# Kernel optimization log

Hardware: AMD Instinct MI355X
Metric: run time of the kernel (lower is better)

Reference implementation:

```python
import jax, jax.numpy as jnp
import numpy as np

N_NODES = 50000
N_EDGES = 625000
D = 128


def setup_inputs() -> dict:
    key = jax.random.key(0)
    kx, ks, kr, kw, kb = jax.random.split(key, 5)
    x = jax.random.normal(kx, (N_NODES, D), dtype=jnp.float32)
    senders = jax.random.randint(ks, (N_EDGES,), 0, N_NODES, dtype=jnp.int64)
    receivers = jax.random.randint(kr, (N_EDGES,), 0, N_NODES, dtype=jnp.int64)
    # nn.Linear(2*D, D): weight [D, 2*D], bias [D]
    lim = 1.0 / np.sqrt(2 * D)
    W = jax.random.uniform(kw, (D, 2 * D), minval=-lim, maxval=lim, dtype=jnp.float32)
    b = jax.random.uniform(kb, (D,), minval=-lim, maxval=lim, dtype=jnp.float32)
    return {"x": x, "senders": senders, "receivers": receivers, "n_nodes": N_NODES, "W": W, "b": b}


def reference(x, senders, receivers, n_nodes, W, b):
    # Add self loops (with_self=True)
    self_idx = jnp.arange(n_nodes, dtype=senders.dtype)
    s = jnp.concatenate([senders, self_idx])   # [E + N]
    r = jnp.concatenate([receivers, self_idx]) # [E + N]

    ones = jnp.ones(r.shape[0], dtype=x.dtype)
    # degree_norm=True branch (note: mirrors the original's naming exactly:
    # 'out_degree' counted over receivers, 'in_degree' over senders)
    out_degree = jax.ops.segment_sum(ones, r, num_segments=n_nodes)  # [N]
    in_degree = jax.ops.segment_sum(ones, s, num_segments=n_nodes)   # [N]
    out_degree_norm = jax.lax.rsqrt(jnp.maximum(out_degree, 1.0))
    in_degree_norm = jax.lax.rsqrt(jnp.maximum(in_degree, 1.0))

    # Gather sender embeddings, scale, scatter-add to receivers
    sender_emb = x[s] * out_degree_norm[s][:, None]  # [E+N, D]
    aggregated = jax.ops.segment_sum(sender_emb, r, num_segments=n_nodes)  # [N, D]

    # edge_count over receivers == out_degree (same scatter), clamped
    edge_count = jnp.maximum(out_degree, 1.0)
    aggregated = aggregated / edge_count[:, None]
    aggregated = aggregated * in_degree_norm[:, None]

    combined = jnp.concatenate([x, aggregated], axis=1)  # [N, 2D]
    return combined @ W.T + b
```

## Files before the change

### kernel.cpp

```cpp
#include <hip/hip_runtime.h>

#define DIM 128
#define BM 128
#define BK 32
#define BINSZ 128
#define EPB 2048

typedef __attribute__((ext_vector_type(8))) short short8;
typedef __attribute__((ext_vector_type(4))) float f32x4;

__device__ __forceinline__ unsigned short f2bf(float f) {
    unsigned int b = __float_as_uint(f);
    return (unsigned short)((b + 0x7fffu + ((b >> 16) & 1u)) >> 16);
}
__device__ __forceinline__ float bf_lo(unsigned int u) { return __uint_as_float(u << 16); }
__device__ __forceinline__ float bf_hi(unsigned int u) { return __uint_as_float(u & 0xffff0000u); }
__device__ __forceinline__ unsigned int pack2(float a, float b) {
    return (unsigned int)f2bf(a) | ((unsigned int)f2bf(b) << 16);
}
__device__ __forceinline__ uint2 pack4(float4 v) {
    uint2 r; r.x = pack2(v.x, v.y); r.y = pack2(v.z, v.w); return r;
}

__global__ void convert_kernel(const float4* __restrict__ x4,
                               const float4* __restrict__ W4,
                               uint2* __restrict__ xb4,
                               uint2* __restrict__ Wb4,
                               int nx4, int nw4) {
    int i = blockIdx.x * blockDim.x + threadIdx.x;
    if (i < nx4) xb4[i] = pack4(x4[i]);
    if (i < nw4) Wb4[i] = pack4(W4[i]);
}

__global__ __launch_bounds__(256) void hist_kernel(
        const int* __restrict__ senders, const int* __restrict__ receivers,
        int* __restrict__ Hr, int* __restrict__ Hs, int E, int nbin) {
    __shared__ int hr[512], hs[512];
    int t = threadIdx.x;
    for (int b = t; b < nbin; b += 256) { hr[b] = 0; hs[b] = 0; }
    __syncthreads();
    int base = blockIdx.x * EPB;
    for (int k = 0; k < EPB; k += 256) {
        int e = base + k + t;
        if (e < E) {
            atomicAdd(&hr[receivers[e] >> 7], 1);
            atomicAdd(&hs[senders[e] >> 7], 1);
        }
    }
    __syncthreads();
    size_t ho = (size_t)blockIdx.x * nbin;
    for (int b = t; b < nbin; b += 256) {
        Hr[ho + b] = hr[b];
        Hs[ho + b] = hs[b];
    }
}

__global__ __launch_bounds__(512) void scan_bins_kernel(
        int* __restrict__ Hr, int* __restrict__ Hs,
        int* __restrict__ tot_r, int* __restrict__ tot_s,
        int NAB, int nbin) {
    __shared__ int sr[512], ss[512];
    int b = blockIdx.x, t = threadIdx.x;
    int vr = (t < NAB) ? Hr[(size_t)t * nbin + b] : 0;
    int vs = (t < NAB) ? Hs[(size_t)t * nbin + b] : 0;
    sr[t] = vr; ss[t] = vs;
    __syncthreads();
    for (int off = 1; off < 512; off <<= 1) {
        int ur = (t >= off) ? sr[t - off] : 0;
        int us = (t >= off) ? ss[t - off] : 0;
        __syncthreads();
        sr[t] += ur; ss[t] += us;
        __syncthreads();
    }
    if (t < NAB) {
        Hr[(size_t)t * nbin + b] = sr[t] - vr;
        Hs[(size_t)t * nbin + b] = ss[t] - vs;
    }
    if (t == 511) { tot_r[b] = sr[511]; tot_s[b] = ss[511]; }
}

__global__ __launch_bounds__(512) void scan_base_kernel(
        const int* __restrict__ tot_r, const int* __restrict__ tot_s,
        int* __restrict__ base_r, int* __restrict__ base_s,
        int* __restrict__ row_start, int nbin, int N, int E) {
    __shared__ int sr[512], ss[512];
    int t = threadIdx.x;
    int vr = (t < nbin) ? tot_r[t] : 0;
    int vs = (t < nbin) ? tot_s[t] : 0;
    sr[t] = vr; ss[t] = vs;
    __syncthreads();
    for (int off = 1; off < 512; off <<= 1) {
        int ur = (t >= off) ? sr[t - off] : 0;
        int us = (t >= off) ? ss[t - off] : 0;
        __syncthreads();
        sr[t] += ur; ss[t] += us;
        __syncthreads();
    }
    if (t < nbin) {
        base_r[t] = sr[t] - vr;
        base_s[t] = ss[t] - vs;
    }
    if (t == 0) { base_r[nbin] = E; base_s[nbin] = E; row_start[N] = E; }
}

__global__ __launch_bounds__(256) void scatter_kernel(
        const int* __restrict__ senders, const int* __restrict__ receivers,
        const int* __restrict__ Hr, const int* __restrict__ Hs,
        const int* __restrict__ base_r, const int* __restrict__ base_s,
        unsigned int* __restrict__ bucket_r, int* __restrict__ bucket_s,
        int E, int nbin) {
    __shared__ int br_[512], bs_[512];
    int t = threadIdx.x;
    size_t ho = (size_t)blockIdx.x * nbin;
    for (int b = t; b < nbin; b += 256) {
        br_[b] = base_r[b] + Hr[ho + b];
        bs_[b] = base_s[b] + Hs[ho + b];
    }
    __syncthreads();
    int base = blockIdx.x * EPB;
    for (int k = 0; k < EPB; k += 256) {
        int e = base + k + t;
        if (e < E) {
            int s = senders[e], r = receivers[e];
            int pr = atomicAdd(&br_[r >> 7], 1);
            bucket_r[pr] = ((unsigned int)(r & 127) << 16) | (unsigned int)s;
            int ps = atomicAdd(&bs_[s >> 7], 1);
            bucket_s[ps] = s;
        }
    }
}

__global__ __launch_bounds__(256) void fine_kernel(
        const unsigned int* __restrict__ bucket_r,
        const int* __restrict__ bucket_s,
        const int* __restrict__ base_r,
        const int* __restrict__ base_s,
        const uint2* __restrict__ xb2,
        int* __restrict__ edge_src,
        int* __restrict__ row_start,
        float* __restrict__ fs,
        uint2* __restrict__ xs2,
        int N) {
    __shared__ int fine[BINSZ], fstart[BINSZ], cs[BINSZ];
    __shared__ float scs[BINSZ];
    int b = blockIdx.x, t = threadIdx.x;
    if (t < BINSZ) { fine[t] = 0; cs[t] = 0; }
    __syncthreads();

    int loR = base_r[b], hiR = base_r[b + 1];
    int loS = base_s[b], hiS = base_s[b + 1];
    for (int i = loR + t; i < hiR; i += 256)
        atomicAdd(&fine[bucket_r[i] >> 16], 1);
    for (int i = loS + t; i < hiS; i += 256)
        atomicAdd(&cs[bucket_s[i] & 127], 1);
    __syncthreads();

    if (t < BINSZ) fstart[t] = fine[t];
    __syncthreads();
    for (int off = 1; off < BINSZ; off <<= 1) {
        int u = (t < BINSZ && t >= off) ? fstart[t - off] : 0;
        __syncthreads();
        if (t < BINSZ) fstart[t] += u;
        __syncthreads();
    }
    if (t < BINSZ) {
        int excl = fstart[t] - fine[t];
        int node = b * BINSZ + t;
        float od = (float)(fine[t] + 1);
        float sc = rsqrtf(od);
        scs[t] = sc;
        if (node < N) {
            row_start[node] = loR + excl;
            fs[node] = rsqrtf((float)(cs[t] + 1)) / od;
        }
        fstart[t] = excl;
    }
    __syncthreads();

    for (int i = loR + t; i < hiR; i += 256) {
        unsigned int u = bucket_r[i];
        int pos = atomicAdd(&fstart[u >> 16], 1);
        edge_src[loR + pos] = (int)(u & 0xFFFFu);
    }

    int nrow0 = b * BINSZ;
    for (int idx = t; idx < BINSZ * 32; idx += 256) {
        int row = idx >> 5, c = idx & 31;
        int node = nrow0 + row;
        if (node < N) {
            float sc = scs[row];
            uint2 u = xb2[(size_t)node * 32 + c];
            uint2 o;
            o.x = pack2(bf_lo(u.x) * sc, bf_hi(u.x) * sc);
            o.y = pack2(bf_lo(u.y) * sc, bf_hi(u.y) * sc);
            xs2[(size_t)node * 32 + c] = o;
        }
    }
}

__global__ __launch_bounds__(256) void gather_kernel(
        const unsigned int* __restrict__ xs,
        const int* __restrict__ edge_src,
        const int* __restrict__ row_start,
        const float* __restrict__ fs,
        unsigned int* __restrict__ aggb,
        int N) {
    int lane = threadIdx.x & 63;
    int n = (blockIdx.x * blockDim.x + threadIdx.x) >> 6;
    if (n >= N) return;

    int start = row_start[n];
    int deg   = row_start[n + 1] - start;
    float ax = 0.f, ay = 0.f;

    for (int base = 0; base < deg; base += 64) {
        int cnt = deg - base; if (cnt > 64) cnt = 64;
        int src = 0;
        if (lane < cnt) src = edge_src[start + base + lane];
        int j = 0;
        for (; j + 8 <= cnt; j += 8) {
            int ss[8]; unsigned int uu[8];
#pragma unroll
            for (int q = 0; q < 8; q++) ss[q] = __shfl(src, j + q);
#pragma unroll
            for (int q = 0; q < 8; q++) uu[q] = xs[(size_t)ss[q] * 64 + lane];
#pragma unroll
            for (int q = 0; q < 8; q++) { ax += bf_lo(uu[q]); ay += bf_hi(uu[q]); }
        }
        for (; j < cnt; j++) {
            int s = __shfl(src, j);
            unsigned int u = xs[(size_t)s * 64 + lane];
            ax += bf_lo(u); ay += bf_hi(u);
        }
    }

    float f = fs[n];
    unsigned int u = xs[(size_t)n * 64 + lane];
    ax = (ax + bf_lo(u)) * f;
    ay = (ay + bf_hi(u)) * f;
    aggb[(size_t)n * 64 + lane] = pack2(ax, ay);
}

__global__ __launch_bounds__(512) void gemm_kernel(
        const unsigned short* __restrict__ x_bf,
        const unsigned short* __restrict__ agg_bf,
        const unsigned short* __restrict__ W_bf,
        const float* __restrict__ bias,
        float* __restrict__ out, int N) {
    __shared__ unsigned short As[BM * BK];
    __shared__ unsigned short Bs[DIM * BK];

    int t    = threadIdx.x;
    int lane = t & 63;
    int w    = t >> 6;
    int wr   = w >> 2, wc = w & 3;
    int row0 = blockIdx.x * BM;

    f32x4 acc[4][2];
#pragma unroll
    for (int i = 0; i < 4; i++)
#pragma unroll
        for (int j = 0; j < 2; j++) acc[i][j] = (f32x4){0.f, 0.f, 0.f, 0.f};

    for (int kt = 0; kt < 8; kt++) {
        const unsigned short* src = (kt < 4) ? x_bf : agg_bf;
        int k0 = (kt & 3) * BK;
        {
            int row = t >> 2, ch = t & 3;
            uint4 v = *(const uint4*)&src[(size_t)(row0 + row) * 128 + k0 + ch * 8];
            *(uint4*)&As[row * BK + ch * 8] = v;
        }
        {
            int n = t >> 2, ch = t & 3;
            uint4 v = *(const uint4*)&W_bf[(size_t)n * 256 + kt * BK + ch * 8];
            *(uint4*)&Bs[n * BK + ch * 8] = v;
        }
        __syncthreads();

        short8 a[4], b[2];
#pragma unroll
        for (int i = 0; i < 4; i++)
            a[i] = *(const short8*)&As[(wr * 64 + i * 16 + (lane & 15)) * BK + (lane >> 4) * 8];
#pragma unroll
        for (int j = 0; j < 2; j++)
            b[j] = *(const short8*)&Bs[(wc * 32 + j * 16 + (lane & 15)) * BK + (lane >> 4) * 8];
#pragma unroll
        for (int i = 0; i < 4; i++)
#pragma unroll
            for (int j = 0; j < 2; j++)
                acc[i][j] = __builtin_amdgcn_mfma_f32_16x16x32_bf16(a[i], b[j], acc[i][j], 0, 0, 0);
        __syncthreads();
    }

    int cq = lane >> 4;
    int cl = lane & 15;
#pragma unroll
    for (int j = 0; j < 2; j++) {
        int col = wc * 32 + j * 16 + cl;
        float bb = bias[col];
#pragma unroll
        for (int i = 0; i < 4; i++) {
            int rbase = row0 + wr * 64 + i * 16 + cq * 4;
#pragma unroll
            for (int r = 0; r < 4; r++) {
                int row = rbase + r;
                if (row < N) out[(size_t)row * DIM + col] = acc[i][j][r] + bb;
            }
        }
    }
}

extern "C" void kernel_launch(void* const* d_in, const int* in_sizes, int n_in,
                              void* d_out, int out_size, void* d_ws, size_t ws_size,
                              hipStream_t stream) {
    const float* x         = (const float*)d_in[0];
    const int*   senders   = (const int*)d_in[1];
    const int*   receivers = (const int*)d_in[2];
    const float* W         = (const float*)d_in[4];
    const float* bias      = (const float*)d_in[5];
    float*       out       = (float*)d_out;

    int N    = in_sizes[0] / DIM;
    int E    = in_sizes[1];
    int nbin = (N + BINSZ - 1) / BINSZ;
    int NAB  = (E + EPB - 1) / EPB;
    int NP   = ((N + BM - 1) / BM) * BM;

    char* ws = (char*)d_ws;
    size_t off = 0;
    #define WS_ALLOC(ptrtype, name, bytes) \
        ptrtype name = (ptrtype)(ws + off); off += (((size_t)(bytes)) + 255) & ~(size_t)255;
    WS_ALLOC(int*,            tot_r,     (size_t)nbin * 4)
    WS_ALLOC(int*,            tot_s,     (size_t)nbin * 4)
    WS_ALLOC(int*,            base_r,    (size_t)(nbin + 1) * 4)
    WS_ALLOC(int*,            base_s,    (size_t)(nbin + 1) * 4)
    WS_ALLOC(int*,            row_start, (size_t)(N + 1) * 4)
    WS_ALLOC(float*,          fs,        (size_t)N * 4)
    WS_ALLOC(int*,            edge_src,  (size_t)E * 4)
    WS_ALLOC(unsigned short*, x_bf,      (size_t)NP * DIM * 2)
    WS_ALLOC(unsigned short*, xs_bf,     (size_t)NP * DIM * 2)
    WS_ALLOC(unsigned short*, agg_bf,    (size_t)NP * DIM * 2)
    WS_ALLOC(unsigned short*, W_bf,      (size_t)DIM * 256 * 2)
    #undef WS_ALLOC

    size_t eb = ((size_t)E * 4 + 255) & ~(size_t)255;
    size_t hb = ((size_t)NAB * nbin * 4 + 255) & ~(size_t)255;
    unsigned int* bucket_r = (unsigned int*)agg_bf;
    int*          bucket_s = (int*)((char*)agg_bf + eb);
    int*          Hr       = (int*)((char*)agg_bf + 2 * eb);
    int*          Hs       = (int*)((char*)agg_bf + 2 * eb + hb);

    int nx4 = N * 32;
    int nw4 = DIM * 256 / 4;
    convert_kernel<<<(nx4 + 255) / 256, 256, 0, stream>>>(
        (const float4*)x, (const float4*)W, (uint2*)x_bf, (uint2*)W_bf, nx4, nw4);
    hist_kernel<<<NAB, 256, 0, stream>>>(senders, receivers, Hr, Hs, E, nbin);
    scan_bins_kernel<<<nbin, 512, 0, stream>>>(Hr, Hs, tot_r, tot_s, NAB, nbin);
    scan_base_kernel<<<1, 512, 0, stream>>>(tot_r, tot_s, base_r, base_s,
                                            row_start, nbin, N, E);
    scatter_kernel<<<NAB, 256, 0, stream>>>(senders, receivers, Hr, Hs,
                                            base_r, base_s, bucket_r, bucket_s, E, nbin);
    fine_kernel<<<nbin, 256, 0, stream>>>(bucket_r, bucket_s, base_r, base_s,
                                          (const uint2*)x_bf, edge_src, row_start,
                                          fs, (uint2*)xs_bf, N);
    gather_kernel<<<(N * 64 + 255) / 256, 256, 0, stream>>>(
        (const unsigned int*)xs_bf, edge_src, row_start, fs,
        (unsigned int*)agg_bf, N);
    gemm_kernel<<<(N + BM - 1) / BM, 512, 0, stream>>>(
        x_bf, agg_bf, W_bf, bias, out, N);
}
```

Measured before the change: 177.7 us.

## Fuse gather into GEMM, merge convert/hist and the two scan kernels

Each GEMM block now gathers its 128 rows of aggregated neighbour features straight into shared memory, so the bf16 aggregate is never written to or read from global memory. The convert and histogram kernels become one launch, and the base scan runs in the last-finishing block of the bin scan, found through an atomic counter. bucket_s is stored as 16-bit indices and the buffers are no longer aliased. The fused kernel runs only 391 blocks of 512 threads with 16 rows per wave done serially, so the gather has much less parallelism and latency hiding than the old per-node launch.

```diff
diff --git a/kernel.cpp b/kernel.cpp
--- a/kernel.cpp
+++ b/kernel.cpp
@@ -5,6 +5,7 @@
 #define BK 32
 #define BINSZ 128
 #define EPB 2048
+#define AGS 136
 
 typedef __attribute__((ext_vector_type(8))) short short8;
 typedef __attribute__((ext_vector_type(4))) float f32x4;
@@ -22,44 +23,44 @@
     uint2 r; r.x = pack2(v.x, v.y); r.y = pack2(v.z, v.w); return r;
 }
 
-__global__ void convert_kernel(const float4* __restrict__ x4,
-                               const float4* __restrict__ W4,
-                               uint2* __restrict__ xb4,
-                               uint2* __restrict__ Wb4,
-                               int nx4, int nw4) {
-    int i = blockIdx.x * blockDim.x + threadIdx.x;
-    if (i < nx4) xb4[i] = pack4(x4[i]);
-    if (i < nw4) Wb4[i] = pack4(W4[i]);
-}
-
-__global__ __launch_bounds__(256) void hist_kernel(
+__global__ __launch_bounds__(256) void convert_hist_kernel(
+        const float4* __restrict__ x4, const float4* __restrict__ W4,
         const int* __restrict__ senders, const int* __restrict__ receivers,
-        int* __restrict__ Hr, int* __restrict__ Hs, int E, int nbin) {
-    __shared__ int hr[512], hs[512];
-    int t = threadIdx.x;
-    for (int b = t; b < nbin; b += 256) { hr[b] = 0; hs[b] = 0; }
-    __syncthreads();
-    int base = blockIdx.x * EPB;
-    for (int k = 0; k < EPB; k += 256) {
-        int e = base + k + t;
-        if (e < E) {
-            atomicAdd(&hr[receivers[e] >> 7], 1);
-            atomicAdd(&hs[senders[e] >> 7], 1);
-        }
-    }
-    __syncthreads();
-    size_t ho = (size_t)blockIdx.x * nbin;
-    for (int b = t; b < nbin; b += 256) {
-        Hr[ho + b] = hr[b];
-        Hs[ho + b] = hs[b];
-    }
-}
-
-__global__ __launch_bounds__(512) void scan_bins_kernel(
+        uint2* __restrict__ xb4, uint2* __restrict__ Wb4,
+        int* __restrict__ Hr, int* __restrict__ Hs, int* __restrict__ done,
+        int nx4, int nw4, int E, int nbin, int NAB) {
+    if ((int)blockIdx.x < NAB) {
+        __shared__ int hr[512], hs[512];
+        int t = threadIdx.x;
+        if (blockIdx.x == 0 && t == 0) *done = 0;
+        for (int b = t; b < nbin; b += 256) { hr[b] = 0; hs[b] = 0; }
+        __syncthreads();
+        int base = blockIdx.x * EPB;
+        for (int k = 0; k < EPB; k += 256) {
+            int e = base + k + t;
+            if (e < E) {
+                atomicAdd(&hr[receivers[e] >> 7], 1);
+                atomicAdd(&hs[senders[e] >> 7], 1);
+            }
+        }
+        __syncthreads();
+        size_t ho = (size_t)blockIdx.x * nbin;
+        for (int b = t; b < nbin; b += 256) { Hr[ho + b] = hr[b]; Hs[ho + b] = hs[b]; }
+    } else {
+        int i = ((int)blockIdx.x - NAB) * 256 + threadIdx.x;
+        if (i < nx4) xb4[i] = pack4(x4[i]);
+        if (i < nw4) Wb4[i] = pack4(W4[i]);
+    }
+}
+
+__global__ __launch_bounds__(512) void scan_kernel(
         int* __restrict__ Hr, int* __restrict__ Hs,
         int* __restrict__ tot_r, int* __restrict__ tot_s,
-        int NAB, int nbin) {
+        int* __restrict__ base_r, int* __restrict__ base_s,
+        int* __restrict__ row_start, int* __restrict__ done,
+        int NAB, int nbin, int N, int E) {
     __shared__ int sr[512], ss[512];
+    __shared__ int rank_sh;
     int b = blockIdx.x, t = threadIdx.x;
     int vr = (t < NAB) ? Hr[(size_t)t * nbin + b] : 0;
     int vs = (t < NAB) ? Hs[(size_t)t * nbin + b] : 0;
@@ -76,38 +77,34 @@
         Hr[(size_t)t * nbin + b] = sr[t] - vr;
         Hs[(size_t)t * nbin + b] = ss[t] - vs;
     }
-    if (t == 511) { tot_r[b] = sr[511]; tot_s[b] = ss[511]; }
-}
-
-__global__ __launch_bounds__(512) void scan_base_kernel(
-        const int* __restrict__ tot_r, const int* __restrict__ tot_s,
-        int* __restrict__ base_r, int* __restrict__ base_s,
-        int* __restrict__ row_start, int nbin, int N, int E) {
-    __shared__ int sr[512], ss[512];
-    int t = threadIdx.x;
-    int vr = (t < nbin) ? tot_r[t] : 0;
-    int vs = (t < nbin) ? tot_s[t] : 0;
-    sr[t] = vr; ss[t] = vs;
-    __syncthreads();
-    for (int off = 1; off < 512; off <<= 1) {
-        int ur = (t >= off) ? sr[t - off] : 0;
-        int us = (t >= off) ? ss[t - off] : 0;
-        __syncthreads();
-        sr[t] += ur; ss[t] += us;
-        __syncthreads();
-    }
-    if (t < nbin) {
-        base_r[t] = sr[t] - vr;
-        base_s[t] = ss[t] - vs;
-    }
-    if (t == 0) { base_r[nbin] = E; base_s[nbin] = E; row_start[N] = E; }
+    if (t == 511) {
+        tot_r[b] = sr[511]; tot_s[b] = ss[511];
+        __threadfence();
+        rank_sh = atomicAdd(done, 1);
+    }
+    __syncthreads();
+    if (rank_sh == (int)gridDim.x - 1) {
+        int wr2 = (t < nbin) ? atomicAdd(&tot_r[t], 0) : 0;
+        int ws2 = (t < nbin) ? atomicAdd(&tot_s[t], 0) : 0;
+        sr[t] = wr2; ss[t] = ws2;
+        __syncthreads();
+        for (int off = 1; off < 512; off <<= 1) {
+            int ur = (t >= off) ? sr[t - off] : 0;
+            int us = (t >= off) ? ss[t - off] : 0;
+            __syncthreads();
+            sr[t] += ur; ss[t] += us;
+            __syncthreads();
+        }
+        if (t < nbin) { base_r[t] = sr[t] - wr2; base_s[t] = ss[t] - ws2; }
+        if (t == 0) { base_r[nbin] = E; base_s[nbin] = E; row_start[N] = E; }
+    }
 }
 
 __global__ __launch_bounds__(256) void scatter_kernel(
         const int* __restrict__ senders, const int* __restrict__ receivers,
         const int* __restrict__ Hr, const int* __restrict__ Hs,
         const int* __restrict__ base_r, const int* __restrict__ base_s,
-        unsigned int* __restrict__ bucket_r, int* __restrict__ bucket_s,
+        unsigned int* __restrict__ bucket_r, unsigned short* __restrict__ bucket_s,
         int E, int nbin) {
     __shared__ int br_[512], bs_[512];
     int t = threadIdx.x;
@@ -125,14 +122,14 @@
             int pr = atomicAdd(&br_[r >> 7], 1);
             bucket_r[pr] = ((unsigned int)(r & 127) << 16) | (unsigned int)s;
             int ps = atomicAdd(&bs_[s >> 7], 1);
-            bucket_s[ps] = s;
+            bucket_s[ps] = (unsigned short)s;
         }
     }
 }
 
 __global__ __launch_bounds__(256) void fine_kernel(
         const unsigned int* __restrict__ bucket_r,
-        const int* __restrict__ bucket_s,
+        const unsigned short* __restrict__ bucket_s,
         const int* __restrict__ base_r,
         const int* __restrict__ base_s,
         const uint2* __restrict__ xb2,
@@ -198,64 +195,59 @@
     }
 }
 
-__global__ __launch_bounds__(256) void gather_kernel(
+__global__ __launch_bounds__(512) void gather_gemm_kernel(
+        const unsigned short* __restrict__ x_bf,
         const unsigned int* __restrict__ xs,
         const int* __restrict__ edge_src,
         const int* __restrict__ row_start,
         const float* __restrict__ fs,
-        unsigned int* __restrict__ aggb,
-        int N) {
-    int lane = threadIdx.x & 63;
-    int n = (blockIdx.x * blockDim.x + threadIdx.x) >> 6;
-    if (n >= N) return;
-
-    int start = row_start[n];
-    int deg   = row_start[n + 1] - start;
-    float ax = 0.f, ay = 0.f;
-
-    for (int base = 0; base < deg; base += 64) {
-        int cnt = deg - base; if (cnt > 64) cnt = 64;
-        int src = 0;
-        if (lane < cnt) src = edge_src[start + base + lane];
-        int j = 0;
-        for (; j + 8 <= cnt; j += 8) {
-            int ss[8]; unsigned int uu[8];
-#pragma unroll
-            for (int q = 0; q < 8; q++) ss[q] = __shfl(src, j + q);
-#pragma unroll
-            for (int q = 0; q < 8; q++) uu[q] = xs[(size_t)ss[q] * 64 + lane];
-#pragma unroll
-            for (int q = 0; q < 8; q++) { ax += bf_lo(uu[q]); ay += bf_hi(uu[q]); }
-        }
-        for (; j < cnt; j++) {
-            int s = __shfl(src, j);
-            unsigned int u = xs[(size_t)s * 64 + lane];
-            ax += bf_lo(u); ay += bf_hi(u);
-        }
-    }
-
-    float f = fs[n];
-    unsigned int u = xs[(size_t)n * 64 + lane];
-    ax = (ax + bf_lo(u)) * f;
-    ay = (ay + bf_hi(u)) * f;
-    aggb[(size_t)n * 64 + lane] = pack2(ax, ay);
-}
-
-__global__ __launch_bounds__(512) void gemm_kernel(
-        const unsigned short* __restrict__ x_bf,
-        const unsigned short* __restrict__ agg_bf,
         const unsigned short* __restrict__ W_bf,
         const float* __restrict__ bias,
         float* __restrict__ out, int N) {
+    __shared__ unsigned short Agg[BM * AGS];
     __shared__ unsigned short As[BM * BK];
     __shared__ unsigned short Bs[DIM * BK];
 
-    int t    = threadIdx.x;
-    int lane = t & 63;
-    int w    = t >> 6;
-    int wr   = w >> 2, wc = w & 3;
+    int t = threadIdx.x, lane = t & 63, w = t >> 6;
     int row0 = blockIdx.x * BM;
 
+    for (int i = 0; i < 16; i++) {
+        int row = w * 16 + i;
+        int n = row0 + row;
+        float ax = 0.f, ay = 0.f;
+        if (n < N) {
+            int start = row_start[n];
+            int deg   = row_start[n + 1] - start;
+            for (int base = 0; base < deg; base += 64) {
+                int cnt = deg - base; if (cnt > 64) cnt = 64;
+                int src = 0;
+                if (lane < cnt) src = edge_src[start + base + lane];
+                int j = 0;
+                for (; j + 8 <= cnt; j += 8) {
+                    int ssx[8]; unsigned int uu[8];
+#pragma unroll
+                    for (int q = 0; q < 8; q++) ssx[q] = __shfl(src, j + q);
+#pragma unroll
+                    for (int q = 0; q < 8; q++) uu[q] = xs[(size_t)ssx[q] * 64 + lane];
+#pragma unroll
+                    for (int q = 0; q < 8; q++) { ax += bf_lo(uu[q]); ay += bf_hi(uu[q]); }
+                }
+                for (; j < cnt; j++) {
+                    int s = __shfl(src, j);
+                    unsigned int u = xs[(size_t)s * 64 + lane];
+                    ax += bf_lo(u); ay += bf_hi(u);
+                }
+            }
+            float f = fs[n];
+            unsigned int u = xs[(size_t)n * 64 + lane];
+            ax = (ax + bf_lo(u)) * f;
+            ay = (ay + bf_hi(u)) * f;
+        }
+        *(unsigned int*)&Agg[row * AGS + 2 * lane] = pack2(ax, ay);
+    }
+    __syncthreads();
+
+    int wr = w >> 2, wc = w & 3;
     f32x4 acc[4][2];
 #pragma unroll
     for (int i = 0; i < 4; i++)
@@ -263,32 +255,34 @@
         for (int j = 0; j < 2; j++) acc[i][j] = (f32x4){0.f, 0.f, 0.f, 0.f};
 
     for (int kt = 0; kt < 8; kt++) {
-        const unsigned short* src = (kt < 4) ? x_bf : agg_bf;
-        int k0 = (kt & 3) * BK;
+        if (kt < 4) {
+            int row = t >> 2, ch = t & 3;
+            uint4 v = *(const uint4*)&x_bf[(size_t)(row0 + row) * 128 + kt * BK + ch * 8];
+            *(uint4*)&As[row * BK + ch * 8] = v;
+        }
         {
-            int row = t >> 2, ch = t & 3;
-            uint4 v = *(const uint4*)&src[(size_t)(row0 + row) * 128 + k0 + ch * 8];
-            *(uint4*)&As[row * BK + ch * 8] = v;
-        }
-        {
-            int n = t >> 2, ch = t & 3;
-            uint4 v = *(const uint4*)&W_bf[(size_t)n * 256 + kt * BK + ch * 8];
-            *(uint4*)&Bs[n * BK + ch * 8] = v;
-        }
-        __syncthreads();
-
-        short8 a[4], b[2];
+            int n2 = t >> 2, ch = t & 3;
+            uint4 v = *(const uint4*)&W_bf[(size_t)n2 * 256 + kt * BK + ch * 8];
+            *(uint4*)&Bs[n2 * BK + ch * 8] = v;
+        }
+        __syncthreads();
+
+        short8 a[4], b2[2];
+#pragma unroll
+        for (int i = 0; i < 4; i++) {
+            int arow = wr * 64 + i * 16 + (lane & 15);
+            a[i] = (kt < 4)
+                ? *(const short8*)&As[arow * BK + (lane >> 4) * 8]
+                : *(const short8*)&Agg[arow * AGS + (kt - 4) * 32 + (lane >> 4) * 8];
+        }
+#pragma unroll
+        for (int j = 0; j < 2; j++)
+            b2[j] = *(const short8*)&Bs[(wc * 32 + j * 16 + (lane & 15)) * BK + (lane >> 4) * 8];
 #pragma unroll
         for (int i = 0; i < 4; i++)
-            a[i] = *(const short8*)&As[(wr * 64 + i * 16 + (lane & 15)) * BK + (lane >> 4) * 8];
-#pragma unroll
-        for (int j = 0; j < 2; j++)
-            b[j] = *(const short8*)&Bs[(wc * 32 + j * 16 + (lane & 15)) * BK + (lane >> 4) * 8];
-#pragma unroll
-        for (int i = 0; i < 4; i++)
 #pragma unroll
             for (int j = 0; j < 2; j++)
-                acc[i][j] = __builtin_amdgcn_mfma_f32_16x16x32_bf16(a[i], b[j], acc[i][j], 0, 0, 0);
+                acc[i][j] = __builtin_amdgcn_mfma_f32_16x16x32_bf16(a[i], b2[j], acc[i][j], 0, 0, 0);
         __syncthreads();
     }
 
@@ -336,36 +330,32 @@
     WS_ALLOC(int*,            base_s,    (size_t)(nbin + 1) * 4)
     WS_ALLOC(int*,            row_start, (size_t)(N + 1) * 4)
     WS_ALLOC(float*,          fs,        (size_t)N * 4)
+    WS_ALLOC(int*,            done,      256)
     WS_ALLOC(int*,            edge_src,  (size_t)E * 4)
     WS_ALLOC(unsigned short*, x_bf,      (size_t)NP * DIM * 2)
     WS_ALLOC(unsigned short*, xs_bf,     (size_t)NP * DIM * 2)
-    WS_ALLOC(unsigned short*, agg_bf,    (size_t)NP * DIM * 2)
     WS_ALLOC(unsigned short*, W_bf,      (size_t)DIM * 256 * 2)
+    WS_ALLOC(unsigned int*,   bucket_r,  (size_t)E * 4)
+    WS_ALLOC(unsigned short*, bucket_s,  (size_t)E * 2)
+    WS_ALLOC(int*,            Hr,        (size_t)NAB * nbin * 4)
+    WS_ALLOC(int*,            Hs,        (size_t)NAB * nbin * 4)
     #undef WS_ALLOC
-
-    size_t eb = ((size_t)E * 4 + 255) & ~(size_t)255;
-    size_t hb = ((size_t)NAB * nbin * 4 + 255) & ~(size_t)255;
-    unsigned int* bucket_r = (unsigned int*)agg_bf;
-    int*          bucket_s = (int*)((char*)agg_bf + eb);
-    int*          Hr       = (int*)((char*)agg_bf + 2 * eb);
-    int*          Hs       = (int*)((char*)agg_bf + 2 * eb + hb);
 
     int nx4 = N * 32;
     int nw4 = DIM * 256 / 4;
-    convert_kernel<<<(nx4 + 255) / 256, 256, 0, stream>>>(
-        (const float4*)x, (const float4*)W, (uint2*)x_bf, (uint2*)W_bf, nx4, nw4);
-    hist_kernel<<<NAB, 256, 0, stream>>>(senders, receivers, Hr, Hs, E, nbin);
-    scan_bins_kernel<<<nbin, 512, 0, stream>>>(Hr, Hs, tot_r, tot_s, NAB, nbin);
-    scan_base_kernel<<<1, 512, 0, stream>>>(tot_r, tot_s, base_r, base_s,
-                                            row_start, nbin, N, E);
+    int conv_blocks = (nx4 + 255) / 256;
+
+    convert_hist_kernel<<<NAB + conv_blocks, 256, 0, stream>>>(
+        (const float4*)x, (const float4*)W, senders, receivers,
+        (uint2*)x_bf, (uint2*)W_bf, Hr, Hs, done, nx4, nw4, E, nbin, NAB);
+    scan_kernel<<<nbin, 512, 0, stream>>>(Hr, Hs, tot_r, tot_s, base_r, base_s,
+                                          row_start, done, NAB, nbin, N, E);
     scatter_kernel<<<NAB, 256, 0, stream>>>(senders, receivers, Hr, Hs,
                                             base_r, base_s, bucket_r, bucket_s, E, nbin);
     fine_kernel<<<nbin, 256, 0, stream>>>(bucket_r, bucket_s, base_r, base_s,
                                           (const uint2*)x_bf, edge_src, row_start,
                                           fs, (uint2*)xs_bf, N);
-    gather_kernel<<<(N * 64 + 255) / 256, 256, 0, stream>>>(
-        (const unsigned int*)xs_bf, edge_src, row_start, fs,
-        (unsigned int*)agg_bf, N);
-    gemm_kernel<<<(N + BM - 1) / BM, 512, 0, stream>>>(
-        x_bf, agg_bf, W_bf, bias, out, N);
-}
+    gather_gemm_kernel<<<(N + BM - 1) / BM, 512, 0, stream>>>(
+        x_bf, (const unsigned int*)xs_bf, edge_src, row_start, fs,
+        W_bf, bias, out, N);
+}
```

Result: slower. 206.3 us (+16.1%).
